# Performance work log

Measured on AMD Instinct MI355X. Metric: run time of the kernel, lower is better.

## Reference

```python
import jax, jax.numpy as jnp
import numpy as np

D = 1024   # d_model
H = 16     # n_heads
S = 2048   # seq_len
HD = D // H  # head_dim = 64
B = 1


def setup_inputs() -> dict:
    key = jax.random.key(0)
    ks = jax.random.split(key, 10)
    s = 0.02
    return {
        "x": jax.random.normal(ks[0], (B, S * D), dtype=jnp.float32),
        "Wq": jax.random.normal(ks[1], (D, D), dtype=jnp.float32) * s,
        "bq": jnp.zeros((D,), dtype=jnp.float32),
        "Wk": jax.random.normal(ks[2], (D, D), dtype=jnp.float32) * s,
        "bk": jnp.zeros((D,), dtype=jnp.float32),
        "Wv": jax.random.normal(ks[3], (D, D), dtype=jnp.float32) * s,
        "bv": jnp.zeros((D,), dtype=jnp.float32),
        "Wo": jax.random.normal(ks[4], (D, D), dtype=jnp.float32) * s,
        "bo": jnp.zeros((D,), dtype=jnp.float32),
        "rel_table": jax.random.normal(ks[5], (2 * S - 1, HD), dtype=jnp.float32),
    }


def reference(x, Wq, bq, Wk, bk, Wv, bv, Wo, bo, rel_table):
    b = x.shape[0]
    x3 = x.reshape(b, S, D)
    # projections; split into heads -> [b, H, S, HD]
    def heads(t):
        return t.reshape(b, S, H, HD).transpose(0, 2, 1, 3)
    Q = heads(x3 @ Wq + bq)
    K = heads(x3 @ Wk + bk)
    V = heads(x3 @ Wv + bv)

    scores = jnp.einsum('bhid,bhjd->bhij', Q, K) / np.sqrt(HD).astype(np.float32)

    # relative position index: clamp(i - j + S - 1, 0, 2S-2)
    pos = jnp.arange(S)
    idx = jnp.clip(pos[:, None] - pos[None, :] + S - 1, 0, 2 * S - 2)  # [S, S]
    # contract Q with the raw table once, then gather per (i, j)
    # (same math as einsum('bhid,ijd->bhij', Q, table[idx]) but avoids [S,S,HD])
    qrel = jnp.einsum('bhid,rd->bhir', Q, rel_table)          # [b, H, S, 2S-1]
    rel_scores = jnp.take_along_axis(qrel, idx[None, None, :, :], axis=-1)  # [b,H,S,S]

    attn = jax.nn.softmax(scores + rel_scores, axis=-1)
    # dropout is identity in eval mode
    out = jnp.einsum('bhij,bhjd->bhid', attn, V)              # [b, H, S, HD]
    out = out.transpose(0, 2, 1, 3).reshape(b, S, D)
    return (out @ Wo + bo).reshape(b, -1)
```

## Files before the change

kernel.cpp:

```cpp
#include <hip/hip_runtime.h>
#include <hip/hip_bf16.h>

#define SEQ 2048
#define DM  1024
#define NH  16
#define HDM 64

typedef __hip_bfloat16 bf16;
typedef __bf16 bhalf8 __attribute__((ext_vector_type(8)));
typedef float floatx4 __attribute__((ext_vector_type(4)));

__device__ __forceinline__ void async_cp16(const void* g, void* l) {
  __builtin_amdgcn_global_load_lds(
      (const __attribute__((address_space(1))) void*)g,
      (__attribute__((address_space(3))) void*)l, 16, 0, 0);
}

__global__ __launch_bounds__(256) void prep(
    const float* __restrict__ x, const float* __restrict__ T,
    const float* __restrict__ W0, const float* __restrict__ W1,
    const float* __restrict__ W2, const float* __restrict__ W3,
    bf16* __restrict__ xbf, bf16* __restrict__ Tbf, bf16* __restrict__ WtBase)
{
  __shared__ float tile[64][69];
  const int b = blockIdx.x;
  const int tid = threadIdx.x;
  if (b < 2048) {
    int c = b * 256 + tid;
    float4 v = *(const float4*)&x[(size_t)c * 4];
    union { bf16 h[4]; float2 f; } u;
    u.h[0] = __float2bfloat16(v.x); u.h[1] = __float2bfloat16(v.y);
    u.h[2] = __float2bfloat16(v.z); u.h[3] = __float2bfloat16(v.w);
    *(float2*)&xbf[(size_t)c * 4] = u.f;
  } else if (b < 2304) {
    int ct = (b - 2048) * 256 + tid;
    union { bf16 h[4]; float2 f; } u;
#pragma unroll
    for (int e = 0; e < 4; ++e) {
      int se = ct * 4 + e;
      if (se >= 4095 * 64) se -= 64;
      u.h[e] = __float2bfloat16(T[se]);
    }
    *(float2*)&Tbf[(size_t)ct * 4] = u.f;
  } else {
    int tb = b - 2304;
    int z = tb >> 8, rem = tb & 255;
    const float* W = (z == 0) ? W0 : (z == 1) ? W1 : (z == 2) ? W2 : W3;
    bf16* Wt = WtBase + (size_t)z * DM * DM;
    const int kb = (rem >> 4) * 64, nb = (rem & 15) * 64;
    const int r = tid >> 4, c4 = (tid & 15) * 4;
#pragma unroll
    for (int rr = 0; rr < 4; ++rr) {
      float4 v = *(const float4*)&W[(size_t)(kb + rr * 16 + r) * DM + nb + c4];
      tile[rr * 16 + r][c4 + 0] = v.x; tile[rr * 16 + r][c4 + 1] = v.y;
      tile[rr * 16 + r][c4 + 2] = v.z; tile[rr * 16 + r][c4 + 3] = v.w;
    }
    __syncthreads();
    const int w = tid >> 6, l = tid & 63;
#pragma unroll
    for (int i = 0; i < 16; ++i) {
      int n = nb + w * 16 + i;
      Wt[(size_t)n * DM + kb + l] = __float2bfloat16(tile[l][w * 16 + i]);
    }
  }
}

__device__ __forceinline__ void gemm64_core(
    const bf16* __restrict__ A, const bf16* __restrict__ Bt,
    bf16* As, bf16* Bs, int bm, int bn, floatx4 (&acc)[4])
{
  const int tid = threadIdx.x;
  const int lane = tid & 63;
  const int w = tid >> 6;
  const int ln15 = lane & 15, quad = lane >> 4;

  for (int k0 = 0; k0 < DM; k0 += 64) {
    {
      int c = w * 64 + lane;
      int row = c >> 2, col = (c & 3) * 8;
      async_cp16(A  + (size_t)(bm + row) * DM + k0 + col,      As + c * 8);
      async_cp16(A  + (size_t)(bm + row) * DM + k0 + 32 + col, As + 2048 + c * 8);
      async_cp16(Bt + (size_t)(bn + row) * DM + k0 + col,      Bs + c * 8);
      async_cp16(Bt + (size_t)(bn + row) * DM + k0 + 32 + col, Bs + 2048 + c * 8);
    }
    __syncthreads();
#pragma unroll
    for (int kk = 0; kk < 2; ++kk) {
      bhalf8 af = *(bhalf8*)&As[kk * 2048 + (w * 16 + ln15) * 32 + quad * 8];
      bhalf8 bfr[4];
#pragma unroll
      for (int j = 0; j < 4; ++j)
        bfr[j] = *(bhalf8*)&Bs[kk * 2048 + (j * 16 + ln15) * 32 + quad * 8];
#pragma unroll
      for (int j = 0; j < 4; ++j)
        acc[j] = __builtin_amdgcn_mfma_f32_16x16x32_bf16(af, bfr[j], acc[j], 0, 0, 0);
    }
    __syncthreads();
  }
}

__global__ __launch_bounds__(256) void gemm_qkv(
    const bf16* __restrict__ A, const bf16* __restrict__ Wt3,
    const float* __restrict__ bq, const float* __restrict__ bk,
    const float* __restrict__ bv, bf16* __restrict__ outbase)
{
  __shared__ __align__(16) bf16 As[64 * 64];
  __shared__ __align__(16) bf16 Bs[64 * 64];
  const int z = blockIdx.z;
  const bf16* Bt = Wt3 + (size_t)z * DM * DM;
  const float* bias = (z == 0) ? bq : (z == 1) ? bk : bv;
  bf16* C = outbase + (size_t)z * SEQ * DM;
  const int bm = blockIdx.y * 64, bn = blockIdx.x * 64;
  floatx4 acc[4];
#pragma unroll
  for (int j = 0; j < 4; ++j) acc[j] = (floatx4){0.f, 0.f, 0.f, 0.f};
  gemm64_core(A, Bt, As, Bs, bm, bn, acc);

  const int lane = threadIdx.x & 63;
  const int w = threadIdx.x >> 6;
  const int ln15 = lane & 15, quad = lane >> 4;
#pragma unroll
  for (int j = 0; j < 4; ++j) {
    int col = bn + j * 16 + ln15;
    float bv_ = bias[col];
#pragma unroll
    for (int r = 0; r < 4; ++r) {
      int row = bm + w * 16 + quad * 4 + r;
      float v = acc[j][r] + bv_;
      if (z < 2)
        C[((size_t)(col >> 6) * SEQ + row) * HDM + (col & 63)] = __float2bfloat16(v);
      else
        C[(size_t)col * SEQ + row] = __float2bfloat16(v);
    }
  }
}

__global__ __launch_bounds__(256) void gemm_out(
    const bf16* __restrict__ A, const bf16* __restrict__ Bt,
    const float* __restrict__ bias, float* __restrict__ C)
{
  __shared__ __align__(16) bf16 As[64 * 64];
  __shared__ __align__(16) bf16 Bs[64 * 64];
  const int bm = blockIdx.y * 64, bn = blockIdx.x * 64;
  floatx4 acc[4];
#pragma unroll
  for (int j = 0; j < 4; ++j) acc[j] = (floatx4){0.f, 0.f, 0.f, 0.f};
  gemm64_core(A, Bt, As, Bs, bm, bn, acc);

  const int lane = threadIdx.x & 63;
  const int w = threadIdx.x >> 6;
  const int ln15 = lane & 15, quad = lane >> 4;
#pragma unroll
  for (int j = 0; j < 4; ++j) {
    int col = bn + j * 16 + ln15;
    float bv_ = bias[col];
#pragma unroll
    for (int r = 0; r < 4; ++r) {
      int row = bm + w * 16 + quad * 4 + r;
      C[(size_t)row * DM + col] = acc[j][r] + bv_;
    }
  }
}

__global__ __launch_bounds__(256, 3) void attn_flash(
    const bf16* __restrict__ Q, const bf16* __restrict__ K,
    const bf16* __restrict__ Vt, const bf16* __restrict__ Tb,
    bf16* __restrict__ Opart, float* __restrict__ ml)
{
  const int i0   = blockIdx.x * 64;
  const int h    = blockIdx.y;
  const int z    = blockIdx.z;
  const int tid  = threadIdx.x;
  const int lane = tid & 63;
  const int wrow = (tid >> 6) * 16;
  const int ln15 = lane & 15;
  const int quad = lane >> 4;

  __shared__ __align__(16) unsigned char smem[44544];
  bf16*  Ks  = (bf16*)smem;
  bf16*  Vs  = (bf16*)(smem + 9216);
  bf16*  Ps  = (bf16*)(smem + 18432);
  float* S2c = (float*)(smem + 27648);
  bf16*  Qs  = (bf16*)(smem + 27648);

  const bf16* Qg = Q  + ((size_t)h * SEQ + i0) * HDM;
  const bf16* Kg = K  + (size_t)h * SEQ * HDM;
  const bf16* Vg = Vt + (size_t)h * HDM * SEQ;

#pragma unroll
  for (int t = 0; t < 2; ++t) {
    int id = tid + t * 256;
    int r = id >> 3, c = (id & 7) * 8;
    *(float4*)&Qs[r * 72 + c] = *(const float4*)&Qg[(size_t)r * HDM + c];
  }
  __syncthreads();

  const bhalf8 aq0 = *(bhalf8*)&Qs[(wrow + ln15) * 72 + quad * 8];
  const bhalf8 aq1 = *(bhalf8*)&Qs[(wrow + ln15) * 72 + quad * 8 + 32];

  floatx4 o[4];
  float mrow[4], lrow[4];
#pragma unroll
  for (int c = 0; c < 4; ++c) o[c] = (floatx4){0.f, 0.f, 0.f, 0.f};
#pragma unroll
  for (int r = 0; r < 4; ++r) { mrow[r] = -1e30f; lrow[r] = 0.f; }

  const int jt0 = z * 16;
  const int rb0 = i0 - jt0 * 64 + SEQ - HDM;
  floatx4 carry[4];
#pragma unroll
  for (int ct = 0; ct < 4; ++ct) {
    const bf16* tr = Tb + (size_t)(rb0 + 64 + ct * 16 + ln15) * HDM + quad * 8;
    bhalf8 b0 = *(const bhalf8*)tr;
    bhalf8 b1 = *(const bhalf8*)(tr + 32);
    floatx4 a = (floatx4){0.f, 0.f, 0.f, 0.f};
    a = __builtin_amdgcn_mfma_f32_16x16x32_bf16(aq0, b0, a, 0, 0, 0);
    a = __builtin_amdgcn_mfma_f32_16x16x32_bf16(aq1, b1, a, 0, 0, 0);
    carry[ct] = a;
  }
  bhalf8 tA[4], tB[4];
#pragma unroll
  for (int ct = 0; ct < 4; ++ct) {
    const bf16* tr = Tb + (size_t)(rb0 + ct * 16 + ln15) * HDM + quad * 8;
    tA[ct] = *(const bhalf8*)tr;
    tB[ct] = *(const bhalf8*)(tr + 32);
  }

  for (int jt = jt0; jt < jt0 + 16; ++jt) {
    const int j0 = jt * 64;
    __syncthreads();
#pragma unroll
    for (int t = 0; t < 2; ++t) {
      int id = tid + t * 256;
      int r = id >> 3, c = (id & 7) * 8;
      *(float4*)&Ks[r * 72 + c] = *(const float4*)&Kg[(size_t)(j0 + r) * HDM + c];
      *(float4*)&Vs[r * 72 + c] = *(const float4*)&Vg[(size_t)r * SEQ + j0 + c];
    }
    __syncthreads();

    floatx4 fresh[4];
#pragma unroll
    for (int ct = 0; ct < 4; ++ct) {
      floatx4 a = (floatx4){0.f, 0.f, 0.f, 0.f};
      a = __builtin_amdgcn_mfma_f32_16x16x32_bf16(aq0, tA[ct], a, 0, 0, 0);
      a = __builtin_amdgcn_mfma_f32_16x16x32_bf16(aq1, tB[ct], a, 0, 0, 0);
      fresh[ct] = a;
    }
    {
      int rnext = i0 - j0 - 64 + SEQ - HDM;
#pragma unroll
      for (int ct = 0; ct < 4; ++ct) {
        const bf16* tr = Tb + (size_t)(rnext + ct * 16 + ln15) * HDM + quad * 8;
        tA[ct] = *(const bhalf8*)tr;
        tB[ct] = *(const bhalf8*)(tr + 32);
      }
    }
#pragma unroll
    for (int ct = 0; ct < 4; ++ct) {
      int t = ct * 16 + ln15;
#pragma unroll
      for (int r = 0; r < 4; ++r) {
        int row = wrow + quad * 4 + r;
        if (t >= row) S2c[row * 66 + (row + 63 - t)] = fresh[ct][r];
        else          S2c[row * 66 + (row - 1 - t)] = carry[ct][r];
      }
      carry[ct] = fresh[ct];
    }

    float sc[4][4];
#pragma unroll
    for (int ct = 0; ct < 4; ++ct) {
      bhalf8 b0 = *(bhalf8*)&Ks[(ct * 16 + ln15) * 72 + quad * 8];
      bhalf8 b1 = *(bhalf8*)&Ks[(ct * 16 + ln15) * 72 + quad * 8 + 32];
      floatx4 a = (floatx4){0.f, 0.f, 0.f, 0.f};
      a = __builtin_amdgcn_mfma_f32_16x16x32_bf16(aq0, b0, a, 0, 0, 0);
      a = __builtin_amdgcn_mfma_f32_16x16x32_bf16(aq1, b1, a, 0, 0, 0);
#pragma unroll
      for (int r = 0; r < 4; ++r) {
        int row = wrow + quad * 4 + r;
        sc[ct][r] = a[r] * 0.125f + S2c[row * 66 + ct * 16 + ln15];
      }
    }
#pragma unroll
    for (int r = 0; r < 4; ++r) {
      float tm = fmaxf(fmaxf(sc[0][r], sc[1][r]), fmaxf(sc[2][r], sc[3][r]));
      tm = fmaxf(tm, __shfl_xor(tm, 1));
      tm = fmaxf(tm, __shfl_xor(tm, 2));
      tm = fmaxf(tm, __shfl_xor(tm, 4));
      tm = fmaxf(tm, __shfl_xor(tm, 8));
      float mn = fmaxf(mrow[r], tm);
      float alpha = __expf(mrow[r] - mn);
      mrow[r] = mn;
      float rs = 0.f;
#pragma unroll
      for (int ct = 0; ct < 4; ++ct) {
        float p = __expf(sc[ct][r] - mn);
        sc[ct][r] = p;
        rs += p;
      }
      rs += __shfl_xor(rs, 1); rs += __shfl_xor(rs, 2);
      rs += __shfl_xor(rs, 4); rs += __shfl_xor(rs, 8);
      lrow[r] = lrow[r] * alpha + rs;
#pragma unroll
      for (int ct = 0; ct < 4; ++ct) o[ct][r] *= alpha;
    }
#pragma unroll
    for (int ct = 0; ct < 4; ++ct)
#pragma unroll
      for (int r = 0; r < 4; ++r)
        Ps[(wrow + quad * 4 + r) * 72 + ct * 16 + ln15] = __float2bfloat16(sc[ct][r]);

    bhalf8 ap0 = *(bhalf8*)&Ps[(wrow + ln15) * 72 + quad * 8];
    bhalf8 ap1 = *(bhalf8*)&Ps[(wrow + ln15) * 72 + quad * 8 + 32];
#pragma unroll
    for (int ct = 0; ct < 4; ++ct) {
      bhalf8 b0 = *(bhalf8*)&Vs[(ct * 16 + ln15) * 72 + quad * 8];
      bhalf8 b1 = *(bhalf8*)&Vs[(ct * 16 + ln15) * 72 + quad * 8 + 32];
      o[ct] = __builtin_amdgcn_mfma_f32_16x16x32_bf16(ap0, b0, o[ct], 0, 0, 0);
      o[ct] = __builtin_amdgcn_mfma_f32_16x16x32_bf16(ap1, b1, o[ct], 0, 0, 0);
    }
  }

  bf16* Oz = Opart + (size_t)z * SEQ * DM;
#pragma unroll
  for (int r = 0; r < 4; ++r) {
    float inv = 1.f / lrow[r];
    int row = i0 + wrow + quad * 4 + r;
#pragma unroll
    for (int ct = 0; ct < 4; ++ct)
      Oz[(size_t)row * DM + h * HDM + ct * 16 + ln15] =
          __float2bfloat16(o[ct][r] * inv);
    if (ln15 == 0) {
      float* mlp = ml + (((size_t)z * NH + h) * SEQ + row) * 2;
      mlp[0] = mrow[r];
      mlp[1] = lrow[r];
    }
  }
}

__global__ __launch_bounds__(256) void attn_merge(
    const bf16* __restrict__ O0, const bf16* __restrict__ O1,
    const float* __restrict__ ml, bf16* __restrict__ O)
{
  const int i = blockIdx.x;
  const int tid = threadIdx.x;
  __shared__ float w0s[NH], w1s[NH];
  if (tid < NH) {
    const float* p0 = ml + (((size_t)0 * NH + tid) * SEQ + i) * 2;
    const float* p1 = ml + (((size_t)1 * NH + tid) * SEQ + i) * 2;
    float m0 = p0[0], l0 = p0[1], m1 = p1[0], l1 = p1[1];
    float m = fmaxf(m0, m1);
    float a = l0 * __expf(m0 - m), b = l1 * __expf(m1 - m);
    float inv = 1.f / (a + b);
    w0s[tid] = a * inv; w1s[tid] = b * inv;
  }
  __syncthreads();
  const int d = tid * 4;
  const float w0 = w0s[d >> 6], w1 = w1s[d >> 6];
  union { bf16 h[4]; float2 f; } a0, a1, ov;
  a0.f = *(const float2*)&O0[(size_t)i * DM + d];
  a1.f = *(const float2*)&O1[(size_t)i * DM + d];
#pragma unroll
  for (int e = 0; e < 4; ++e)
    ov.h[e] = __float2bfloat16(w0 * __bfloat162float(a0.h[e]) +
                               w1 * __bfloat162float(a1.h[e]));
  *(float2*)&O[(size_t)i * DM + d] = ov.f;
}

extern "C" void kernel_launch(void* const* d_in, const int* in_sizes, int n_in,
                              void* d_out, int out_size, void* d_ws, size_t ws_size,
                              hipStream_t stream) {
  const float* x   = (const float*)d_in[0];
  const float* Wq  = (const float*)d_in[1];
  const float* bq  = (const float*)d_in[2];
  const float* Wk  = (const float*)d_in[3];
  const float* bk  = (const float*)d_in[4];
  const float* Wv  = (const float*)d_in[5];
  const float* bv  = (const float*)d_in[6];
  const float* Wo  = (const float*)d_in[7];
  const float* bo  = (const float*)d_in[8];
  const float* rel = (const float*)d_in[9];
  float* out = (float*)d_out;

  const size_t SD = (size_t)SEQ * DM;
  bf16* qws = (bf16*)d_ws;
  bf16* kws = qws + SD;
  bf16* vws = kws + SD;
  bf16* ows = vws + SD;
  bf16* xbf = ows + SD;
  bf16* wt  = xbf + SD;
  bf16* tbfBase = wt + 4 * (size_t)DM * DM;
  bf16* tbf = tbfBase + (size_t)64 * HDM;
  bf16* opart = tbf + (size_t)4096 * HDM;
  float* ml   = (float*)(opart + 2 * SD);

  prep<<<3328, 256, 0, stream>>>(x, rel, Wq, Wk, Wv, Wo, xbf, tbf, wt);
  gemm_qkv<<<dim3(16, 32, 3), 256, 0, stream>>>(xbf, wt, bq, bk, bv, qws);
  attn_flash<<<dim3(SEQ / 64, NH, 2), 256, 0, stream>>>(qws, kws, vws, tbf,
                                                        opart, ml);
  attn_merge<<<SEQ, 256, 0, stream>>>(opart, opart + SD, ml, ows);
  gemm_out<<<dim3(16, 32), 256, 0, stream>>>(ows, wt + 3 * (size_t)DM * DM, bo, out);
}
```

Before: 236.1 us.

## Stage K, V and rel-table tiles via async global-to-LDS loads and fold scale into K

The 1/sqrt(d) scale is moved into the K projection epilogue. The attention kernel now loads K, V and the relative-table tile straight into LDS with global_load_lds in a split-half layout, replacing register-staged copies and the per-lane table prefetch. The relative-score buffer is stored transposed so each lane can read a float4 and use it as the MFMA accumulator init, which removes the separate scale-and-add. LDS use grows, which may reduce occupancy, and the table base pointer offset changes, so negative table indices now need checking.

```diff
diff --git a/kernel.cpp b/kernel.cpp
--- a/kernel.cpp
+++ b/kernel.cpp
@@ -109,6 +109,7 @@
   const int z = blockIdx.z;
   const bf16* Bt = Wt3 + (size_t)z * DM * DM;
   const float* bias = (z == 0) ? bq : (z == 1) ? bk : bv;
+  const float kscale = (z == 1) ? 0.125f : 1.0f;
   bf16* C = outbase + (size_t)z * SEQ * DM;
   const int bm = blockIdx.y * 64, bn = blockIdx.x * 64;
   floatx4 acc[4];
@@ -126,7 +127,7 @@
 #pragma unroll
     for (int r = 0; r < 4; ++r) {
       int row = bm + w * 16 + quad * 4 + r;
-      float v = acc[j][r] + bv_;
+      float v = (acc[j][r] + bv_) * kscale;
       if (z < 2)
         C[((size_t)(col >> 6) * SEQ + row) * HDM + (col & 63)] = __float2bfloat16(v);
       else
@@ -176,12 +177,13 @@
   const int ln15 = lane & 15;
   const int quad = lane >> 4;
 
-  __shared__ __align__(16) unsigned char smem[44544];
+  __shared__ __align__(16) unsigned char smem[51200];
   bf16*  Ks  = (bf16*)smem;
-  bf16*  Vs  = (bf16*)(smem + 9216);
-  bf16*  Ps  = (bf16*)(smem + 18432);
-  float* S2c = (float*)(smem + 27648);
-  bf16*  Qs  = (bf16*)(smem + 27648);
+  bf16*  Vs  = (bf16*)(smem + 8192);
+  bf16*  Ts  = (bf16*)(smem + 16384);
+  bf16*  Ps  = (bf16*)(smem + 24576);
+  float* S2t = (float*)(smem + 33792);
+  bf16*  Qs  = (bf16*)(smem + 33792);
 
   const bf16* Qg = Q  + ((size_t)h * SEQ + i0) * HDM;
   const bf16* Kg = K  + (size_t)h * SEQ * HDM;
@@ -218,68 +220,53 @@
     a = __builtin_amdgcn_mfma_f32_16x16x32_bf16(aq1, b1, a, 0, 0, 0);
     carry[ct] = a;
   }
-  bhalf8 tA[4], tB[4];
-#pragma unroll
-  for (int ct = 0; ct < 4; ++ct) {
-    const bf16* tr = Tb + (size_t)(rb0 + ct * 16 + ln15) * HDM + quad * 8;
-    tA[ct] = *(const bhalf8*)tr;
-    tB[ct] = *(const bhalf8*)(tr + 32);
-  }
+
+  const int r4 = tid >> 2, c8 = (tid & 3) * 8;
 
   for (int jt = jt0; jt < jt0 + 16; ++jt) {
     const int j0 = jt * 64;
-    __syncthreads();
-#pragma unroll
-    for (int t = 0; t < 2; ++t) {
-      int id = tid + t * 256;
-      int r = id >> 3, c = (id & 7) * 8;
-      *(float4*)&Ks[r * 72 + c] = *(const float4*)&Kg[(size_t)(j0 + r) * HDM + c];
-      *(float4*)&Vs[r * 72 + c] = *(const float4*)&Vg[(size_t)r * SEQ + j0 + c];
-    }
+    const int rbase = i0 - j0 + SEQ - HDM;
+    __syncthreads();
+    async_cp16(Kg + (size_t)(j0 + r4) * HDM + c8,        Ks + tid * 8);
+    async_cp16(Kg + (size_t)(j0 + r4) * HDM + 32 + c8,   Ks + 2048 + tid * 8);
+    async_cp16(Vg + (size_t)r4 * SEQ + j0 + c8,          Vs + tid * 8);
+    async_cp16(Vg + (size_t)r4 * SEQ + j0 + 32 + c8,     Vs + 2048 + tid * 8);
+    async_cp16(Tb + (size_t)(rbase + r4) * HDM + c8,     Ts + tid * 8);
+    async_cp16(Tb + (size_t)(rbase + r4) * HDM + 32 + c8, Ts + 2048 + tid * 8);
     __syncthreads();
 
     floatx4 fresh[4];
 #pragma unroll
     for (int ct = 0; ct < 4; ++ct) {
-      floatx4 a = (floatx4){0.f, 0.f, 0.f, 0.f};
-      a = __builtin_amdgcn_mfma_f32_16x16x32_bf16(aq0, tA[ct], a, 0, 0, 0);
-      a = __builtin_amdgcn_mfma_f32_16x16x32_bf16(aq1, tB[ct], a, 0, 0, 0);
-      fresh[ct] = a;
-    }
-    {
-      int rnext = i0 - j0 - 64 + SEQ - HDM;
-#pragma unroll
-      for (int ct = 0; ct < 4; ++ct) {
-        const bf16* tr = Tb + (size_t)(rnext + ct * 16 + ln15) * HDM + quad * 8;
-        tA[ct] = *(const bhalf8*)tr;
-        tB[ct] = *(const bhalf8*)(tr + 32);
-      }
-    }
-#pragma unroll
-    for (int ct = 0; ct < 4; ++ct) {
-      int t = ct * 16 + ln15;
-#pragma unroll
-      for (int r = 0; r < 4; ++r) {
-        int row = wrow + quad * 4 + r;
-        if (t >= row) S2c[row * 66 + (row + 63 - t)] = fresh[ct][r];
-        else          S2c[row * 66 + (row - 1 - t)] = carry[ct][r];
-      }
-      carry[ct] = fresh[ct];
-    }
-
-    float sc[4][4];
-#pragma unroll
-    for (int ct = 0; ct < 4; ++ct) {
-      bhalf8 b0 = *(bhalf8*)&Ks[(ct * 16 + ln15) * 72 + quad * 8];
-      bhalf8 b1 = *(bhalf8*)&Ks[(ct * 16 + ln15) * 72 + quad * 8 + 32];
+      bhalf8 b0 = *(bhalf8*)&Ts[(ct * 16 + ln15) * 32 + quad * 8];
+      bhalf8 b1 = *(bhalf8*)&Ts[2048 + (ct * 16 + ln15) * 32 + quad * 8];
       floatx4 a = (floatx4){0.f, 0.f, 0.f, 0.f};
       a = __builtin_amdgcn_mfma_f32_16x16x32_bf16(aq0, b0, a, 0, 0, 0);
       a = __builtin_amdgcn_mfma_f32_16x16x32_bf16(aq1, b1, a, 0, 0, 0);
+      fresh[ct] = a;
+    }
+#pragma unroll
+    for (int ct = 0; ct < 4; ++ct) {
+      int t = ct * 16 + ln15;
 #pragma unroll
       for (int r = 0; r < 4; ++r) {
         int row = wrow + quad * 4 + r;
-        sc[ct][r] = a[r] * 0.125f + S2c[row * 66 + ct * 16 + ln15];
+        if (t >= row) S2t[(row + 63 - t) * 68 + row] = fresh[ct][r];
+        else          S2t[(row - 1 - t) * 68 + row] = carry[ct][r];
       }
+      carry[ct] = fresh[ct];
+    }
+
+    float sc[4][4];
+#pragma unroll
+    for (int ct = 0; ct < 4; ++ct) {
+      floatx4 s2f = *(floatx4*)&S2t[(ct * 16 + ln15) * 68 + wrow + quad * 4];
+      bhalf8 b0 = *(bhalf8*)&Ks[(ct * 16 + ln15) * 32 + quad * 8];
+      bhalf8 b1 = *(bhalf8*)&Ks[2048 + (ct * 16 + ln15) * 32 + quad * 8];
+      floatx4 a = __builtin_amdgcn_mfma_f32_16x16x32_bf16(aq0, b0, s2f, 0, 0, 0);
+      a = __builtin_amdgcn_mfma_f32_16x16x32_bf16(aq1, b1, a, 0, 0, 0);
+#pragma unroll
+      for (int r = 0; r < 4; ++r) sc[ct][r] = a[r];
     }
 #pragma unroll
     for (int r = 0; r < 4; ++r) {
@@ -314,8 +301,8 @@
     bhalf8 ap1 = *(bhalf8*)&Ps[(wrow + ln15) * 72 + quad * 8 + 32];
 #pragma unroll
     for (int ct = 0; ct < 4; ++ct) {
-      bhalf8 b0 = *(bhalf8*)&Vs[(ct * 16 + ln15) * 72 + quad * 8];
-      bhalf8 b1 = *(bhalf8*)&Vs[(ct * 16 + ln15) * 72 + quad * 8 + 32];
+      bhalf8 b0 = *(bhalf8*)&Vs[(ct * 16 + ln15) * 32 + quad * 8];
+      bhalf8 b1 = *(bhalf8*)&Vs[2048 + (ct * 16 + ln15) * 32 + quad * 8];
       o[ct] = __builtin_amdgcn_mfma_f32_16x16x32_bf16(ap0, b0, o[ct], 0, 0, 0);
       o[ct] = __builtin_amdgcn_mfma_f32_16x16x32_bf16(ap1, b1, o[ct], 0, 0, 0);
     }
@@ -389,8 +376,7 @@
   bf16* ows = vws + SD;
   bf16* xbf = ows + SD;
   bf16* wt  = xbf + SD;
-  bf16* tbfBase = wt + 4 * (size_t)DM * DM;
-  bf16* tbf = tbfBase + (size_t)64 * HDM;
+  bf16* tbf = wt + 4 * (size_t)DM * DM;
   bf16* opart = tbf + (size_t)4096 * HDM;
   float* ml   = (float*)(opart + 2 * SD);
 
```

After: 226.7 us. -4.0%, faster.
